# Performance work log

Hardware: AMD Instinct MI355X
Metric: run time of the kernel (lower is better)

The kernel has to match this reference:

```python
import jax, jax.numpy as jnp
import numpy as np

NEG_INF = -1e9  # stands in for the -inf diagonal mask of criss-cross attention
BN_EPS = 1e-5


def conv1x1(x, w, b=None):
    # x: [B,Cin,H,W], w: [Cout,Cin]
    y = jnp.einsum('bchw,oc->bohw', x, w)
    if b is not None:
        y = y + b[None, :, None, None]
    return y


def criss_cross(qf, kf, vf, q_w, q_b, k_w, k_b, v_w, v_b, gamma):
    # Criss-cross attention (CCNet): row + column affinity, joint softmax, aggregate.
    B, C, H, W = vf.shape
    q = conv1x1(qf, q_w, q_b)  # [B,Ci,H,W]
    k = conv1x1(kf, k_w, k_b)  # [B,Ci,H,W]
    v = conv1x1(vf, v_w, v_b)  # [B,C,H,W]
    # column-wise (along H) energy, with -inf on the self position (h == h')
    eH = jnp.einsum('bchw,bcHw->bhwH', q, k)
    eH = eH + NEG_INF * jnp.eye(H, dtype=eH.dtype)[:, None, :]  # [H,1,H] broadcasts over w
    # row-wise (along W) energy
    eW = jnp.einsum('bchw,bchW->bhwW', q, k)
    att = jax.nn.softmax(jnp.concatenate([eH, eW], axis=-1), axis=-1)  # [B,H,W,H+W]
    aH, aW = att[..., :H], att[..., H:]
    outH = jnp.einsum('bcHw,bhwH->bchw', v, aH)
    outW = jnp.einsum('bchW,bhwW->bchw', v, aW)
    return gamma * (outH + outW) + vf


def batchnorm(x, scale, bias):
    # training-mode BN over (N,H,W)
    mean = x.mean(axis=(0, 2, 3), keepdims=True)
    var = x.var(axis=(0, 2, 3), keepdims=True)
    xh = (x - mean) * jax.lax.rsqrt(var + BN_EPS)
    return xh * scale[None, :, None, None] + bias[None, :, None, None]


def setup_inputs() -> dict:
    key = jax.random.key(0)
    ks = jax.random.split(key, 16)
    B, C, H, W = 8, 512, 96, 96
    Hh, Wh = 48, 48
    Cin = C // 2    # 256
    Ci = C // 16    # 32
    s = 0.02
    inp = {
        'low_feature': jax.random.normal(ks[0], (B, C, H, W), jnp.float32),
        'high_feature': jax.random.normal(ks[1], (B, C, Hh, Wh), jnp.float32),
        'conv1_w': jax.random.normal(ks[2], (Cin, C), jnp.float32) * s,
        'conv1_b': jnp.zeros((Cin,), jnp.float32),
        'conv2_w': jax.random.normal(ks[3], (Cin, C), jnp.float32) * s,
        'conv2_b': jnp.zeros((Cin,), jnp.float32),
        'q_w': jax.random.normal(ks[4], (Ci, Cin), jnp.float32) * s,
        'q_b': jnp.zeros((Ci,), jnp.float32),
        'k_w': jax.random.normal(ks[5], (Ci, Cin), jnp.float32) * s,
        'k_b': jnp.zeros((Ci,), jnp.float32),
        'v_w': jax.random.normal(ks[6], (Cin, Cin), jnp.float32) * s,
        'v_b': jnp.zeros((Cin,), jnp.float32),
        'gamma': jnp.array(0.1, jnp.float32),
        'bottleneck_w': jax.random.normal(ks[7], (C, Cin + C), jnp.float32) * s,
        'bn_scale': jnp.ones((C,), jnp.float32),
        'bn_bias': jnp.zeros((C,), jnp.float32),
    }
    return inp


def reference(low_feature, high_feature, conv1_w, conv1_b, conv2_w, conv2_b,
              q_w, q_b, k_w, k_b, v_w, v_b, gamma, bottleneck_w, bn_scale, bn_bias):
    B, C, H, W = low_feature.shape
    hf = jax.image.resize(high_feature, (B, high_feature.shape[1], H, W), method='bilinear')
    qf = conv1x1(low_feature, conv1_w, conv1_b)   # [B,C/2,H,W]
    vf = conv1x1(hf, conv2_w, conv2_b)            # [B,C/2,H,W]
    for _ in range(2):  # module applies the same attention twice
        vf = criss_cross(qf, vf, vf, q_w, q_b, k_w, k_b, v_w, v_b, gamma)
    cat = jnp.concatenate([vf, hf], axis=1)       # [B, C/2 + C, H, W]
    out = conv1x1(cat, bottleneck_w)              # bias=False
    out = batchnorm(out, bn_scale, bn_bias)
    return jax.nn.relu(out)
```

## Files before the change

### kernel.cpp

```cpp
#include <hip/hip_runtime.h>
#include <hip/hip_bf16.h>

typedef __hip_bfloat16 bf16;
typedef __attribute__((ext_vector_type(8))) short short8;
typedef __attribute__((ext_vector_type(4))) float f32x4;

constexpr int kHW = 96 * 96;

__device__ __forceinline__ float b2f(bf16 x){ return __bfloat162float(x); }
__device__ __forceinline__ bf16  f2b(float x){ return __float2bfloat16(x); }
__device__ __forceinline__ unsigned short b2u(bf16 x){ return *(unsigned short*)&x; }

#define SW(r, g) ((r)*32 + ((((g) ^ (((r) >> 1) & 3))) << 3))


__global__ void k_zero(float* __restrict__ p){
  int i = blockIdx.x*256 + threadIdx.x;
  if (i < 1024) p[i] = 0.0f;
}

__global__ void k_cvt(const float* __restrict__ s, bf16* __restrict__ d, int n){
  int i = blockIdx.x*256 + threadIdx.x;
  if (i < n) d[i] = f2b(s[i]);
}

__global__ __launch_bounds__(256) void k_upsample(const float* __restrict__ hi,
                                                  bf16* __restrict__ hf_t){
  int y = blockIdx.x, b = blockIdx.y, t = threadIdx.x;
  int j = y >> 1;
  int j0, j1; float wy0, wy1;
  if ((y & 1) == 0){ j0 = j - 1; if (j0 < 0) j0 = 0; j1 = j; wy0 = 0.25f; wy1 = 0.75f; }
  else             { j0 = j; j1 = j + 1; if (j1 > 47) j1 = 47; wy0 = 0.75f; wy1 = 0.25f; }
  __shared__ __align__(16) float sm[2][128][49];
  for (int c0 = 0; c0 < 512; c0 += 128){
    for (int e = t; e < 2*128*48; e += 256){
      int cl = e / 96; int r = e % 96; int jj = r / 48; int i = r % 48;
      int row = jj ? j1 : j0;
      sm[jj][cl][i] = hi[(((size_t)b*512 + c0 + cl)*48 + row)*48 + i];
    }
    __syncthreads();
    for (int e = t; e < 96*128; e += 256){
      int x = e >> 7; int cl = e & 127;
      int i = x >> 1; int i0, i1; float wx0, wx1;
      if ((x & 1) == 0){ i0 = i - 1; if (i0 < 0) i0 = 0; i1 = i; wx0 = 0.25f; wx1 = 0.75f; }
      else             { i0 = i; i1 = i + 1; if (i1 > 47) i1 = 47; wx0 = 0.75f; wx1 = 0.25f; }
      float v = wy0*(wx0*sm[0][cl][i0] + wx1*sm[0][cl][i1])
              + wy1*(wx0*sm[1][cl][i0] + wx1*sm[1][cl][i1]);
      hf_t[(((size_t)b*96 + x)*96 + y)*512 + c0 + cl] = f2b(v);
    }
    __syncthreads();
  }
}

__global__ void k_qqw(const float* __restrict__ q_w, const float* __restrict__ c1_w,
                      bf16* __restrict__ qq_wb){
  int gid = blockIdx.x*256 + threadIdx.x;
  int o = gid >> 9, c = gid & 511;
  float acc = 0.f;
  for (int k = 0; k < 256; k++) acc += q_w[o*256 + k] * c1_w[k*512 + c];
  qq_wb[gid] = f2b(acc);
}
__global__ void k_qqb(const float* __restrict__ q_w, const float* __restrict__ c1_b,
                      const float* __restrict__ q_b, float* __restrict__ qq_b){
  int o = threadIdx.x; if (o >= 32) return;
  float acc = q_b[o];
  for (int k = 0; k < 256; k++) acc += q_w[o*256 + k] * c1_b[k];
  qq_b[o] = acc;
}

__global__ __launch_bounds__(256) void k_mfma_gemm(const bf16* __restrict__ A,
                                                   const bf16* __restrict__ Wb,
                                                   const float* __restrict__ bias,
                                                   bf16* __restrict__ out,
                                                   int K, int O){
  int b = blockIdx.z, n0 = blockIdx.x*128, o0 = blockIdx.y*128;
  int t = threadIdx.x, lane = t & 63, wv = t >> 6;
  int m_off = (wv & 1)*64, o_off = (wv >> 1)*64;
  int lm = lane & 15, lk = lane >> 4;
  __shared__ __align__(16) bf16 As[2][128*32];
  __shared__ __align__(16) bf16 Ws[2][128*32];
  f32x4 acc[4][4] = {};
  const bf16* Ab = A + (size_t)b*kHW*K;
  int nl0 = t >> 2, gp = t & 3, p0 = gp*8;
  uint4 pa0, pa1, pw0, pw1;
  pa0 = *(const uint4*)&Ab[(size_t)(n0+nl0)*K + p0];
  pa1 = *(const uint4*)&Ab[(size_t)(n0+nl0+64)*K + p0];
  pw0 = *(const uint4*)&Wb[(size_t)(o0+nl0)*K + p0];
  pw1 = *(const uint4*)&Wb[(size_t)(o0+nl0+64)*K + p0];
  *(uint4*)&As[0][SW(nl0, gp)]    = pa0;
  *(uint4*)&As[0][SW(nl0+64, gp)] = pa1;
  *(uint4*)&Ws[0][SW(nl0, gp)]    = pw0;
  *(uint4*)&Ws[0][SW(nl0+64, gp)] = pw1;
  int cur = 0;
  int NS = K >> 5;
  for (int s = 0; s < NS; s++){
    if (s+1 < NS){
      int c0 = (s+1)*32;
      pa0 = *(const uint4*)&Ab[(size_t)(n0+nl0)*K + c0 + p0];
      pa1 = *(const uint4*)&Ab[(size_t)(n0+nl0+64)*K + c0 + p0];
      pw0 = *(const uint4*)&Wb[(size_t)(o0+nl0)*K + c0 + p0];
      pw1 = *(const uint4*)&Wb[(size_t)(o0+nl0+64)*K + c0 + p0];
    }
    __syncthreads();
    short8 af[4], bfr[4];
    #pragma unroll
    for (int i = 0; i < 4; i++){
      af[i]  = *(const short8*)&As[cur][SW(m_off + i*16 + lm, lk)];
      bfr[i] = *(const short8*)&Ws[cur][SW(o_off + i*16 + lm, lk)];
    }
    #pragma unroll
    for (int i = 0; i < 4; i++)
      #pragma unroll
      for (int j = 0; j < 4; j++)
        acc[i][j] = __builtin_amdgcn_mfma_f32_16x16x32_bf16(af[i], bfr[j], acc[i][j], 0, 0, 0);
    if (s+1 < NS){
      int nx = cur ^ 1;
      *(uint4*)&As[nx][SW(nl0, gp)]    = pa0;
      *(uint4*)&As[nx][SW(nl0+64, gp)] = pa1;
      *(uint4*)&Ws[nx][SW(nl0, gp)]    = pw0;
      *(uint4*)&Ws[nx][SW(nl0+64, gp)] = pw1;
      cur = nx;
    }
  }
  #pragma unroll
  for (int j = 0; j < 4; j++){
    int oc = o0 + o_off + j*16 + lm;
    float bs = bias ? bias[oc] : 0.0f;
    #pragma unroll
    for (int i = 0; i < 4; i++){
      int rbase = n0 + m_off + i*16 + lk*4;
      #pragma unroll
      for (int r = 0; r < 4; r++)
        out[((size_t)b*kHW + rbase + r)*(size_t)O + oc] = f2b(acc[i][j][r] + bs);
    }
  }
}

__global__ __launch_bounds__(256) void k_bneck_mfma(const bf16* __restrict__ vf,
                                                    const bf16* __restrict__ hf,
                                                    const bf16* __restrict__ Wb,
                                                    bf16* __restrict__ out,
                                                    float* __restrict__ s1,
                                                    float* __restrict__ s2){
  int b = blockIdx.z, n0 = blockIdx.x*128, o0 = blockIdx.y*128;
  int t = threadIdx.x, lane = t & 63, wv = t >> 6;
  int m_off = (wv & 1)*64, o_off = (wv >> 1)*64;
  int lm = lane & 15, lk = lane >> 4;
  __shared__ __align__(16) bf16 As[2][128*32];
  __shared__ __align__(16) bf16 Ws[2][128*32];
  __shared__ float l1[128];
  __shared__ float l2[128];
  if (t < 128){ l1[t] = 0.f; l2[t] = 0.f; }
  f32x4 acc[4][4] = {};
  int nl0 = t >> 2, gp = t & 3, p0 = gp*8;
  const bf16* vfb = vf + (size_t)b*kHW*256;
  const bf16* hfb = hf + (size_t)b*kHW*512;
  uint4 pa0, pa1, pw0, pw1;
  pa0 = *(const uint4*)&vfb[(size_t)(n0+nl0)*256 + p0];
  pa1 = *(const uint4*)&vfb[(size_t)(n0+nl0+64)*256 + p0];
  pw0 = *(const uint4*)&Wb[(size_t)(o0+nl0)*768 + p0];
  pw1 = *(const uint4*)&Wb[(size_t)(o0+nl0+64)*768 + p0];
  *(uint4*)&As[0][SW(nl0, gp)]    = pa0;
  *(uint4*)&As[0][SW(nl0+64, gp)] = pa1;
  *(uint4*)&Ws[0][SW(nl0, gp)]    = pw0;
  *(uint4*)&Ws[0][SW(nl0+64, gp)] = pw1;
  int cur = 0;
  for (int s = 0; s < 24; s++){
    if (s+1 < 24){
      int c0 = (s+1)*32;
      if (c0 < 256){
        pa0 = *(const uint4*)&vfb[(size_t)(n0+nl0)*256 + c0 + p0];
        pa1 = *(const uint4*)&vfb[(size_t)(n0+nl0+64)*256 + c0 + p0];
      } else {
        int cc = c0 - 256;
        pa0 = *(const uint4*)&hfb[(size_t)(n0+nl0)*512 + cc + p0];
        pa1 = *(const uint4*)&hfb[(size_t)(n0+nl0+64)*512 + cc + p0];
      }
      pw0 = *(const uint4*)&Wb[(size_t)(o0+nl0)*768 + c0 + p0];
      pw1 = *(const uint4*)&Wb[(size_t)(o0+nl0+64)*768 + c0 + p0];
    }
    __syncthreads();
    short8 af[4], bfr[4];
    #pragma unroll
    for (int i = 0; i < 4; i++){
      af[i]  = *(const short8*)&As[cur][SW(m_off + i*16 + lm, lk)];
      bfr[i] = *(const short8*)&Ws[cur][SW(o_off + i*16 + lm, lk)];
    }
    #pragma unroll
    for (int i = 0; i < 4; i++)
      #pragma unroll
      for (int j = 0; j < 4; j++)
        acc[i][j] = __builtin_amdgcn_mfma_f32_16x16x32_bf16(af[i], bfr[j], acc[i][j], 0, 0, 0);
    if (s+1 < 24){
      int nx = cur ^ 1;
      *(uint4*)&As[nx][SW(nl0, gp)]    = pa0;
      *(uint4*)&As[nx][SW(nl0+64, gp)] = pa1;
      *(uint4*)&Ws[nx][SW(nl0, gp)]    = pw0;
      *(uint4*)&Ws[nx][SW(nl0+64, gp)] = pw1;
      cur = nx;
    }
  }
  #pragma unroll
  for (int j = 0; j < 4; j++){
    int oc = o0 + o_off + j*16 + lm;
    float p1 = 0.f, p2 = 0.f;
    #pragma unroll
    for (int i = 0; i < 4; i++){
      int rbase = n0 + m_off + i*16 + lk*4;
      #pragma unroll
      for (int r = 0; r < 4; r++){
        float v = acc[i][j][r];
        p1 += v; p2 += v*v;
        out[((size_t)b*kHW + rbase + r)*512 + oc] = f2b(v);
      }
    }
    int cl = o_off + j*16 + lm;
    atomicAdd(&l1[cl], p1);
    atomicAdd(&l2[cl], p2);
  }
  __syncthreads();
  if (t < 128){
    atomicAdd(&s1[o0 + t], l1[t]);
    atomicAdd(&s2[o0 + t], l2[t]);
  }
}

__global__ __launch_bounds__(256) void k_qmfma(const float* __restrict__ low,
                                               const bf16* __restrict__ qq_wb,
                                               const float* __restrict__ qq_b,
                                               bf16* __restrict__ q_t){
  int n0 = blockIdx.x*64, b = blockIdx.y, t = threadIdx.x;
  int lane = t & 63, wv = t >> 6;
  int m_off = wv*16;
  int lm = lane & 15, lk = lane >> 4;
  __shared__ __align__(16) bf16 As[64*36];
  __shared__ __align__(16) bf16 Ws[32*40];
  f32x4 acc[2] = {};
  const float* low_b = low + (size_t)b*512*kHW;
  int c2 = (t & 15)*2;
  int xg = t >> 4;
  for (int c0 = 0; c0 < 512; c0 += 32){
    const float* p0 = low_b + (size_t)(c0 + c2)*kHW + n0 + xg*4;
    float4 a0 = *(const float4*)p0;
    float4 a1 = *(const float4*)(p0 + kHW);
    float f0[4] = {a0.x, a0.y, a0.z, a0.w};
    float f1[4] = {a1.x, a1.y, a1.z, a1.w};
    #pragma unroll
    for (int u = 0; u < 4; u++){
      ushort2 pr;
      bf16 v0 = f2b(f0[u]), v1 = f2b(f1[u]);
      pr.x = b2u(v0); pr.y = b2u(v1);
      *(ushort2*)&As[(xg*4 + u)*36 + c2] = pr;
    }
    if (t < 128){
      int ol = t >> 2, p = t & 3;
      *(uint4*)&Ws[ol*40 + p*8] = *(const uint4*)&qq_wb[(size_t)ol*512 + c0 + p*8];
    }
    __syncthreads();
    short8 af = *(const short8*)&As[(m_off + lm)*36 + lk*8];
    short8 b0 = *(const short8*)&Ws[lm*40 + lk*8];
    short8 b1 = *(const short8*)&Ws[(16 + lm)*40 + lk*8];
    acc[0] = __builtin_amdgcn_mfma_f32_16x16x32_bf16(af, b0, acc[0], 0, 0, 0);
    acc[1] = __builtin_amdgcn_mfma_f32_16x16x32_bf16(af, b1, acc[1], 0, 0, 0);
    __syncthreads();
  }
  #pragma unroll
  for (int j = 0; j < 2; j++){
    int oc = j*16 + lm;
    float bs = qq_b[oc];
    #pragma unroll
    for (int r = 0; r < 4; r++){
      int ng = n0 + m_off + lk*4 + r;
      int h = ng / 96, x = ng - h*96;
      q_t[(((size_t)b*96 + x)*96 + h)*32 + oc] = f2b(acc[j][r] + bs);
    }
  }
}

__global__ __launch_bounds__(256) void k_kmfma(const bf16* __restrict__ A,
                                               const bf16* __restrict__ Wk,
                                               const float* __restrict__ bias,
                                               bf16* __restrict__ out){
  int n0 = blockIdx.x*128, b = blockIdx.y;
  int t = threadIdx.x, lane = t & 63, wv = t >> 6;
  int m_off = wv*32;
  int lm = lane & 15, lk = lane >> 4;
  __shared__ __align__(16) bf16 As[2][128*32];
  __shared__ __align__(16) bf16 Ws[2][32*32];
  f32x4 acc[2][2] = {};
  const bf16* Ab = A + (size_t)b*kHW*256;
  int nl0 = t >> 2, gp = t & 3, p0 = gp*8;
  int ol = t >> 2;
  uint4 pa0, pa1, pw;
  pa0 = *(const uint4*)&Ab[(size_t)(n0+nl0)*256 + p0];
  pa1 = *(const uint4*)&Ab[(size_t)(n0+nl0+64)*256 + p0];
  if (t < 128) pw = *(const uint4*)&Wk[(size_t)ol*256 + p0];
  *(uint4*)&As[0][SW(nl0, gp)]    = pa0;
  *(uint4*)&As[0][SW(nl0+64, gp)] = pa1;
  if (t < 128) *(uint4*)&Ws[0][SW(ol, gp)] = pw;
  int cur = 0;
  for (int s = 0; s < 8; s++){
    if (s+1 < 8){
      int c0 = (s+1)*32;
      pa0 = *(const uint4*)&Ab[(size_t)(n0+nl0)*256 + c0 + p0];
      pa1 = *(const uint4*)&Ab[(size_t)(n0+nl0+64)*256 + c0 + p0];
      if (t < 128) pw = *(const uint4*)&Wk[(size_t)ol*256 + c0 + p0];
    }
    __syncthreads();
    short8 af[2], bfr[2];
    #pragma unroll
    for (int i = 0; i < 2; i++)
      af[i] = *(const short8*)&As[cur][SW(m_off + i*16 + lm, lk)];
    #pragma unroll
    for (int j = 0; j < 2; j++)
      bfr[j] = *(const short8*)&Ws[cur][SW(j*16 + lm, lk)];
    #pragma unroll
    for (int i = 0; i < 2; i++)
      #pragma unroll
      for (int j = 0; j < 2; j++)
        acc[i][j] = __builtin_amdgcn_mfma_f32_16x16x32_bf16(af[i], bfr[j], acc[i][j], 0, 0, 0);
    if (s+1 < 8){
      int nx = cur ^ 1;
      *(uint4*)&As[nx][SW(nl0, gp)]    = pa0;
      *(uint4*)&As[nx][SW(nl0+64, gp)] = pa1;
      if (t < 128) *(uint4*)&Ws[nx][SW(ol, gp)] = pw;
      cur = nx;
    }
  }
  #pragma unroll
  for (int j = 0; j < 2; j++){
    int oc = j*16 + lm;
    float bs = bias[oc];
    #pragma unroll
    for (int i = 0; i < 2; i++){
      int rbase = n0 + m_off + i*16 + lk*4;
      #pragma unroll
      for (int r = 0; r < 4; r++)
        out[((size_t)b*kHW + rbase + r)*32 + oc] = f2b(acc[i][j][r] + bs);
    }
  }
}

__global__ __launch_bounds__(256) void k_eH(const bf16* __restrict__ q_t,
                                            const bf16* __restrict__ k_t,
                                            bf16* __restrict__ att){
  int w = blockIdx.x, b = blockIdx.y, t = threadIdx.x;
  __shared__ float Qs[96][33];
  __shared__ float Ks[96][33];
  const bf16* Qp = q_t + (((size_t)b*96 + w)*96)*32;
  const bf16* Kp = k_t + (((size_t)b*96 + w)*96)*32;
  for (int e = t; e < 3072; e += 256){ Qs[e>>5][e&31] = b2f(Qp[e]); Ks[e>>5][e&31] = b2f(Kp[e]); }
  __syncthreads();
  int tj = t % 16, th = t / 16;
  float acc[6][6] = {};
  #pragma unroll 4
  for (int c = 0; c < 32; c++){
    float qa[6], kb[6];
    #pragma unroll
    for (int i = 0; i < 6; i++) qa[i] = Qs[th*6 + i][c];
    #pragma unroll
    for (int jj = 0; jj < 6; jj++) kb[jj] = Ks[tj*6 + jj][c];
    #pragma unroll
    for (int i = 0; i < 6; i++)
      #pragma unroll
      for (int jj = 0; jj < 6; jj++) acc[i][jj] += qa[i]*kb[jj];
  }
  #pragma unroll
  for (int i = 0; i < 6; i++){
    int h = th*6 + i;
    size_t base = (((size_t)b*96 + h)*96 + w)*192;
    #pragma unroll
    for (int jj = 0; jj < 6; jj++){
      int jg = tj*6 + jj;
      float e = acc[i][jj];
      if (jg == h) e += -1000000000.0f;
      att[base + jg] = f2b(e);
    }
  }
}

__global__ __launch_bounds__(256) void k_eW(const bf16* __restrict__ q_t,
                                            const bf16* __restrict__ k_t,
                                            bf16* __restrict__ att){
  int h = blockIdx.x, b = blockIdx.y, t = threadIdx.x;
  __shared__ float Qs[96][33];
  __shared__ float Ks[96][33];
  for (int e = t; e < 3072; e += 256){
    int wl = e >> 5, c = e & 31;
    size_t idx = (((size_t)b*96 + wl)*96 + h)*32 + c;
    Qs[wl][c] = b2f(q_t[idx]);
    Ks[wl][c] = b2f(k_t[idx]);
  }
  __syncthreads();
  int tj = t % 16, tw = t / 16;
  float acc[6][6] = {};
  #pragma unroll 4
  for (int c = 0; c < 32; c++){
    float qa[6], kb[6];
    #pragma unroll
    for (int i = 0; i < 6; i++) qa[i] = Qs[tw*6 + i][c];
    #pragma unroll
    for (int jj = 0; jj < 6; jj++) kb[jj] = Ks[tj*6 + jj][c];
    #pragma unroll
    for (int i = 0; i < 6; i++)
      #pragma unroll
      for (int jj = 0; jj < 6; jj++) acc[i][jj] += qa[i]*kb[jj];
  }
  #pragma unroll
  for (int i = 0; i < 6; i++){
    int wl = tw*6 + i;
    size_t base = (((size_t)b*96 + h)*96 + wl)*192 + 96;
    #pragma unroll
    for (int jj = 0; jj < 6; jj++) att[base + tj*6 + jj] = f2b(acc[i][jj]);
  }
}

__global__ __launch_bounds__(256) void k_softmax(bf16* __restrict__ att){
  int t = threadIdx.x;
  int row = blockIdx.x*4 + (t >> 6);
  int lane = t & 63;
  size_t base = (size_t)row * 192;
  float x0 = b2f(att[base + lane]);
  float x1 = b2f(att[base + 64 + lane]);
  float x2 = b2f(att[base + 128 + lane]);
  float m = fmaxf(x0, fmaxf(x1, x2));
  #pragma unroll
  for (int off = 32; off; off >>= 1) m = fmaxf(m, __shfl_xor(m, off));
  float e0 = __expf(x0 - m), e1 = __expf(x1 - m), e2 = __expf(x2 - m);
  float s = e0 + e1 + e2;
  #pragma unroll
  for (int off = 32; off; off >>= 1) s += __shfl_xor(s, off);
  float inv = 1.0f / s;
  att[base + lane]       = f2b(e0 * inv);
  att[base + 64 + lane]  = f2b(e1 * inv);
  att[base + 128 + lane] = f2b(e2 * inv);
}

__global__ __launch_bounds__(256) void k_outH_mfma(const bf16* __restrict__ att,
                                                   const bf16* __restrict__ v_t,
                                                   bf16* __restrict__ accb){
  int w = blockIdx.x, b = blockIdx.y, t = threadIdx.x;
  int lane = t & 63, wv = t >> 6;
  int m_off = (wv & 1)*48, o_off = (wv >> 1)*128;
  int lm = lane & 15, lk = lane >> 4;
  __shared__ __align__(16) bf16 As[96*36];
  __shared__ __align__(16) bf16 Vt[256*36];
  f32x4 acc[3][8] = {};
  const bf16* Vb = v_t + ((size_t)b*96 + w)*96*256;
  for (int j0 = 0; j0 < 96; j0 += 32){
    for (int e = t; e < 384; e += 256){
      int h = e >> 2, p = e & 3;
      *(uint4*)&As[h*36 + p*8] =
        *(const uint4*)&att[(((size_t)b*96 + h)*96 + w)*192 + j0 + p*8];
    }
    for (int e = t; e < 512; e += 256){
      int jj2 = (e & 15)*2, cg = e >> 4;
      const bf16* p = Vb + (size_t)(j0 + jj2)*256 + cg*8;
      uint4 a0 = *(const uint4*)p;
      uint4 a1 = *(const uint4*)(p + 256);
      const unsigned short* u0 = (const unsigned short*)&a0;
      const unsigned short* u1 = (const unsigned short*)&a1;
      #pragma unroll
      for (int u = 0; u < 8; u++){
        ushort2 pr; pr.x = u0[u]; pr.y = u1[u];
        *(ushort2*)&Vt[(cg*8 + u)*36 + jj2] = pr;
      }
    }
    __syncthreads();
    short8 af[3], bfr[8];
    #pragma unroll
    for (int i = 0; i < 3; i++)
      af[i] = *(const short8*)&As[(m_off + i*16 + lm)*36 + lk*8];
    #pragma unroll
    for (int j = 0; j < 8; j++)
      bfr[j] = *(const short8*)&Vt[(o_off + j*16 + lm)*36 + lk*8];
    #pragma unroll
    for (int i = 0; i < 3; i++)
      #pragma unroll
      for (int j = 0; j < 8; j++)
        acc[i][j] = __builtin_amdgcn_mfma_f32_16x16x32_bf16(af[i], bfr[j], acc[i][j], 0, 0, 0);
    __syncthreads();
  }
  #pragma unroll
  for (int j = 0; j < 8; j++){
    int c = o_off + j*16 + lm;
    #pragma unroll
    for (int i = 0; i < 3; i++){
      int hbase = m_off + i*16 + lk*4;
      #pragma unroll
      for (int r = 0; r < 4; r++)
        accb[(((size_t)b*96 + w)*96 + hbase + r)*256 + c] = f2b(acc[i][j][r]);
    }
  }
}

__global__ __launch_bounds__(256) void k_outW_mfma(const bf16* __restrict__ att,
                                                   const bf16* __restrict__ v_t,
                                                   const bf16* __restrict__ accb,
                                                   const float* __restrict__ gamma_p,
                                                   bf16* __restrict__ vf_t){
  int h = blockIdx.x, b = blockIdx.y, t = threadIdx.x;
  int lane = t & 63, wv = t >> 6;
  int m_off = (wv & 1)*48, o_off = (wv >> 1)*128;
  int lm = lane & 15, lk = lane >> 4;
  __shared__ __align__(16) bf16 As[96*36];
  __shared__ __align__(16) bf16 Vt[256*36];
  f32x4 acc[3][8] = {};
  for (int j0 = 0; j0 < 96; j0 += 32){
    for (int e = t; e < 384; e += 256){
      int wl = e >> 2, p = e & 3;
      *(uint4*)&As[wl*36 + p*8] =
        *(const uint4*)&att[(((size_t)b*96 + h)*96 + wl)*192 + 96 + j0 + p*8];
    }
    for (int e = t; e < 512; e += 256){
      int jj2 = (e & 15)*2, cg = e >> 4;
      const bf16* p = v_t + (((size_t)b*96 + j0 + jj2)*96 + h)*256 + cg*8;
      uint4 a0 = *(const uint4*)p;
      uint4 a1 = *(const uint4*)(p + 96*256);
      const unsigned short* u0 = (const unsigned short*)&a0;
      const unsigned short* u1 = (const unsigned short*)&a1;
      #pragma unroll
      for (int u = 0; u < 8; u++){
        ushort2 pr; pr.x = u0[u]; pr.y = u1[u];
        *(ushort2*)&Vt[(cg*8 + u)*36 + jj2] = pr;
      }
    }
    __syncthreads();
    short8 af[3], bfr[8];
    #pragma unroll
    for (int i = 0; i < 3; i++)
      af[i] = *(const short8*)&As[(m_off + i*16 + lm)*36 + lk*8];
    #pragma unroll
    for (int j = 0; j < 8; j++)
      bfr[j] = *(const short8*)&Vt[(o_off + j*16 + lm)*36 + lk*8];
    #pragma unroll
    for (int i = 0; i < 3; i++)
      #pragma unroll
      for (int j = 0; j < 8; j++)
        acc[i][j] = __builtin_amdgcn_mfma_f32_16x16x32_bf16(af[i], bfr[j], acc[i][j], 0, 0, 0);
    __syncthreads();
  }
  float g = gamma_p[0];
  #pragma unroll
  for (int j = 0; j < 8; j++){
    int c = o_off + j*16 + lm;
    #pragma unroll
    for (int i = 0; i < 3; i++){
      int wbase = m_off + i*16 + lk*4;
      #pragma unroll
      for (int r = 0; r < 4; r++){
        size_t idx = (((size_t)b*96 + wbase + r)*96 + h)*256 + c;
        vf_t[idx] = f2b(b2f(vf_t[idx]) + g*(acc[i][j][r] + b2f(accb[idx])));
      }
    }
  }
}

__global__ void k_bnprep(const float* __restrict__ s1, const float* __restrict__ s2,
                         const float* __restrict__ sc, const float* __restrict__ bi,
                         float2* __restrict__ ab){
  int co = blockIdx.x*256 + threadIdx.x;
  if (co >= 512) return;
  const float N = 73728.0f;
  float mean = s1[co] / N;
  float var  = s2[co] / N - mean*mean;
  if (var < 0.f) var = 0.f;
  float a = rsqrtf(var + 1e-5f) * sc[co];
  ab[co] = make_float2(a, bi[co] - mean*a);
}

__global__ __launch_bounds__(256) void k_bnout(const bf16* __restrict__ bt,
                                               const float2* __restrict__ ab,
                                               float* __restrict__ out){
  int w0 = blockIdx.x*32, h = blockIdx.y, b = blockIdx.z, t = threadIdx.x;
  __shared__ float Tl[32][33];
  for (int co0 = 0; co0 < 512; co0 += 32){
    for (int e = t; e < 1024; e += 256){
      int wl = e >> 5, co = e & 31;
      Tl[wl][co] = b2f(bt[(((size_t)b*96 + w0 + wl)*96 + h)*512 + co0 + co]);
    }
    __syncthreads();
    for (int e = t; e < 1024; e += 256){
      int co = e >> 5, wl = e & 31;
      float2 s = ab[co0 + co];
      float v = fmaxf(Tl[wl][co]*s.x + s.y, 0.0f);
      out[(((size_t)b*512 + co0 + co)*96 + h)*96 + w0 + wl] = v;
    }
    __syncthreads();
  }
}

extern "C" void kernel_launch(void* const* d_in, const int* in_sizes, int n_in,
                              void* d_out, int out_size, void* d_ws, size_t ws_size,
                              hipStream_t stream){
  (void)in_sizes; (void)n_in; (void)out_size; (void)ws_size;
  const float* low   = (const float*)d_in[0];
  const float* high  = (const float*)d_in[1];
  const float* c1w   = (const float*)d_in[2];
  const float* c1b   = (const float*)d_in[3];
  const float* c2w   = (const float*)d_in[4];
  const float* c2b   = (const float*)d_in[5];
  const float* qw    = (const float*)d_in[6];
  const float* qb    = (const float*)d_in[7];
  const float* kw    = (const float*)d_in[8];
  const float* kb    = (const float*)d_in[9];
  const float* vw    = (const float*)d_in[10];
  const float* vb    = (const float*)d_in[11];
  const float* gamma = (const float*)d_in[12];
  const float* bw    = (const float*)d_in[13];
  const float* bns   = (const float*)d_in[14];
  const float* bnb   = (const float*)d_in[15];
  float* out = (float*)d_out;

  char* wsb = (char*)d_ws;
  bf16*   hf_t = (bf16*) (wsb + 0);
  bf16*   vf_t = (bf16*) (wsb + 75497472);
  bf16*   q_t  = (bf16*) (wsb + 113246208);
  bf16*   qq_wb= (bf16*) (wsb + 117964800);
  bf16*   wk   = (bf16*) (wsb + 117997568);
  float*  qq_b = (float*)(wsb + 118030336);
  float*  s1   = (float*)(wsb + 118030464);
  float*  s2   = (float*)(wsb + 118032512);
  float2* ab   = (float2*)(wsb + 118034560);
  bf16*   wbb  = (bf16*) (wsb + 118038656);
  bf16*   wc2  = (bf16*) (wsb + 118825088);
  bf16*   wv   = (bf16*) (wsb + 119087232);
  bf16*   v_t  = (bf16*) (wsb + 119218304);
  bf16*   att  = (bf16*) (wsb + 156967040);
  bf16*   accb = (bf16*) (wsb + 185278592);
  bf16*   k_t  = (bf16*) (wsb + 185278592);
  bf16*   bt   = (bf16*) (wsb + 119218304);

  k_zero<<<4, 256, 0, stream>>>(s1);
  k_cvt<<<1536, 256, 0, stream>>>(bw,  wbb, 393216);
  k_cvt<<<512,  256, 0, stream>>>(c2w, wc2, 131072);
  k_cvt<<<256,  256, 0, stream>>>(vw,  wv,  65536);
  k_cvt<<<32,   256, 0, stream>>>(kw,  wk,  8192);
  k_upsample<<<dim3(96, 8), 256, 0, stream>>>(high, hf_t);
  k_qqw<<<64, 256, 0, stream>>>(qw, c1w, qq_wb);
  k_qqb<<<1, 64, 0, stream>>>(qw, c1b, qb, qq_b);
  k_mfma_gemm<<<dim3(72, 2, 8), 256, 0, stream>>>(hf_t, wc2, c2b, vf_t, 512, 256);
  k_qmfma<<<dim3(144, 8), 256, 0, stream>>>(low, qq_wb, qq_b, q_t);

  for (int r = 0; r < 2; r++){
    k_kmfma<<<dim3(72, 8), 256, 0, stream>>>(vf_t, wk, kb, k_t);
    k_mfma_gemm<<<dim3(72, 2, 8), 256, 0, stream>>>(vf_t, wv, vb, v_t, 256, 256);
    k_eH<<<dim3(96, 8), 256, 0, stream>>>(q_t, k_t, att);
    k_eW<<<dim3(96, 8), 256, 0, stream>>>(q_t, k_t, att);
    k_softmax<<<18432, 256, 0, stream>>>(att);
    k_outH_mfma<<<dim3(96, 8), 256, 0, stream>>>(att, v_t, accb);
    k_outW_mfma<<<dim3(96, 8), 256, 0, stream>>>(att, v_t, accb, gamma, vf_t);
  }

  k_bneck_mfma<<<dim3(72, 4, 8), 256, 0, stream>>>(vf_t, hf_t, wbb, bt, s1, s2);
  k_bnprep<<<2, 256, 0, stream>>>(s1, s2, bns, bnb, ab);
  k_bnout<<<dim3(3, 96, 8), 256, 0, stream>>>(bt, ab, out);
}
```

Measured before the change: 956.3 us.

## Deepen GEMM prefetch pipeline and vectorize bf16 loads in attention and BN kernels

The two MFMA GEMM kernels now unroll the K loop by two with fixed LDS buffers, issuing global loads for A one stage further ahead than the W loads so more memory latency is hidden behind MFMA work. The eH/eW energy kernels switch from scalar bf16 loads to 16-byte short8 loads with bit-shift conversion into padded float4-aligned shared tiles. The BN output kernel loads 8 bf16 per thread with a uint4 and processes 64 channels per iteration. This costs more live registers for the prefetch buffers and changes the shared-memory padding, which could alter bank conflicts in the compute loops.

```diff
diff --git a/kernel.cpp b/kernel.cpp
--- a/kernel.cpp
+++ b/kernel.cpp
@@ -10,8 +10,19 @@
 __device__ __forceinline__ float b2f(bf16 x){ return __bfloat162float(x); }
 __device__ __forceinline__ bf16  f2b(float x){ return __float2bfloat16(x); }
 __device__ __forceinline__ unsigned short b2u(bf16 x){ return *(unsigned short*)&x; }
+__device__ __forceinline__ float s2f(short u){ return __uint_as_float(((unsigned)(unsigned short)u) << 16); }
 
 #define SW(r, g) ((r)*32 + ((((g) ^ (((r) >> 1) & 3))) << 3))
+
+#define MFMA_STEP(cb) do { \
+  short8 af_[4], bf_[4]; \
+  _Pragma("unroll") for (int i_ = 0; i_ < 4; i_++){ \
+    af_[i_] = *(const short8*)&As[cb][SW(m_off + i_*16 + lm, lk)]; \
+    bf_[i_] = *(const short8*)&Ws[cb][SW(o_off + i_*16 + lm, lk)]; } \
+  _Pragma("unroll") for (int i_ = 0; i_ < 4; i_++) \
+    _Pragma("unroll") for (int j_ = 0; j_ < 4; j_++) \
+      acc[i_][j_] = __builtin_amdgcn_mfma_f32_16x16x32_bf16(af_[i_], bf_[j_], acc[i_][j_], 0, 0, 0); \
+} while(0)
 
 
 __global__ void k_zero(float* __restrict__ p){
@@ -82,44 +93,43 @@
   f32x4 acc[4][4] = {};
   const bf16* Ab = A + (size_t)b*kHW*K;
   int nl0 = t >> 2, gp = t & 3, p0 = gp*8;
-  uint4 pa0, pa1, pw0, pw1;
-  pa0 = *(const uint4*)&Ab[(size_t)(n0+nl0)*K + p0];
-  pa1 = *(const uint4*)&Ab[(size_t)(n0+nl0+64)*K + p0];
-  pw0 = *(const uint4*)&Wb[(size_t)(o0+nl0)*K + p0];
-  pw1 = *(const uint4*)&Wb[(size_t)(o0+nl0+64)*K + p0];
-  *(uint4*)&As[0][SW(nl0, gp)]    = pa0;
-  *(uint4*)&As[0][SW(nl0+64, gp)] = pa1;
-  *(uint4*)&Ws[0][SW(nl0, gp)]    = pw0;
-  *(uint4*)&Ws[0][SW(nl0+64, gp)] = pw1;
-  int cur = 0;
+  const bf16* ar0 = Ab + (size_t)(n0+nl0)*K + p0;
+  const bf16* ar1 = Ab + (size_t)(n0+nl0+64)*K + p0;
+  const bf16* wr0 = Wb + (size_t)(o0+nl0)*K + p0;
+  const bf16* wr1 = Wb + (size_t)(o0+nl0+64)*K + p0;
   int NS = K >> 5;
-  for (int s = 0; s < NS; s++){
-    if (s+1 < NS){
-      int c0 = (s+1)*32;
-      pa0 = *(const uint4*)&Ab[(size_t)(n0+nl0)*K + c0 + p0];
-      pa1 = *(const uint4*)&Ab[(size_t)(n0+nl0+64)*K + c0 + p0];
-      pw0 = *(const uint4*)&Wb[(size_t)(o0+nl0)*K + c0 + p0];
-      pw1 = *(const uint4*)&Wb[(size_t)(o0+nl0+64)*K + c0 + p0];
-    }
-    __syncthreads();
-    short8 af[4], bfr[4];
-    #pragma unroll
-    for (int i = 0; i < 4; i++){
-      af[i]  = *(const short8*)&As[cur][SW(m_off + i*16 + lm, lk)];
-      bfr[i] = *(const short8*)&Ws[cur][SW(o_off + i*16 + lm, lk)];
-    }
-    #pragma unroll
-    for (int i = 0; i < 4; i++)
-      #pragma unroll
-      for (int j = 0; j < 4; j++)
-        acc[i][j] = __builtin_amdgcn_mfma_f32_16x16x32_bf16(af[i], bfr[j], acc[i][j], 0, 0, 0);
-    if (s+1 < NS){
-      int nx = cur ^ 1;
-      *(uint4*)&As[nx][SW(nl0, gp)]    = pa0;
-      *(uint4*)&As[nx][SW(nl0+64, gp)] = pa1;
-      *(uint4*)&Ws[nx][SW(nl0, gp)]    = pw0;
-      *(uint4*)&Ws[nx][SW(nl0+64, gp)] = pw1;
-      cur = nx;
+  {
+    uint4 t0 = *(const uint4*)ar0;
+    uint4 t1 = *(const uint4*)ar1;
+    uint4 t2 = *(const uint4*)wr0;
+    uint4 t3 = *(const uint4*)wr1;
+    *(uint4*)&As[0][SW(nl0, gp)]    = t0;
+    *(uint4*)&As[0][SW(nl0+64, gp)] = t1;
+    *(uint4*)&Ws[0][SW(nl0, gp)]    = t2;
+    *(uint4*)&Ws[0][SW(nl0+64, gp)] = t3;
+  }
+  uint4 Aa0, Aa1, Ab0, Ab1, Wx0, Wx1, Wy0, Wy1;
+  Aa0 = *(const uint4*)(ar0 + 32);
+  Aa1 = *(const uint4*)(ar1 + 32);
+  for (int s = 0; s < NS; s += 2){
+    if (s+2 < NS){ Ab0 = *(const uint4*)(ar0 + (s+2)*32); Ab1 = *(const uint4*)(ar1 + (s+2)*32); }
+    Wx0 = *(const uint4*)(wr0 + (s+1)*32);
+    Wx1 = *(const uint4*)(wr1 + (s+1)*32);
+    __syncthreads();
+    MFMA_STEP(0);
+    *(uint4*)&As[1][SW(nl0, gp)]    = Aa0;
+    *(uint4*)&As[1][SW(nl0+64, gp)] = Aa1;
+    *(uint4*)&Ws[1][SW(nl0, gp)]    = Wx0;
+    *(uint4*)&Ws[1][SW(nl0+64, gp)] = Wx1;
+    if (s+3 < NS){ Aa0 = *(const uint4*)(ar0 + (s+3)*32); Aa1 = *(const uint4*)(ar1 + (s+3)*32); }
+    if (s+2 < NS){ Wy0 = *(const uint4*)(wr0 + (s+2)*32); Wy1 = *(const uint4*)(wr1 + (s+2)*32); }
+    __syncthreads();
+    MFMA_STEP(1);
+    if (s+2 < NS){
+      *(uint4*)&As[0][SW(nl0, gp)]    = Ab0;
+      *(uint4*)&As[0][SW(nl0+64, gp)] = Ab1;
+      *(uint4*)&Ws[0][SW(nl0, gp)]    = Wy0;
+      *(uint4*)&Ws[0][SW(nl0+64, gp)] = Wy1;
     }
   }
   #pragma unroll
@@ -134,6 +144,13 @@
         out[((size_t)b*kHW + rbase + r)*(size_t)O + oc] = f2b(acc[i][j][r] + bs);
     }
   }
+}
+
+__device__ __forceinline__ const bf16* bneck_aptr(const bf16* vfb, const bf16* hfb,
+                                                  int nrow, int p0, int s){
+  int c0 = s*32;
+  return (c0 < 256) ? vfb + (size_t)nrow*256 + c0 + p0
+                    : hfb + (size_t)nrow*512 + (c0 - 256) + p0;
 }
 
 __global__ __launch_bounds__(256) void k_bneck_mfma(const bf16* __restrict__ vf,
@@ -155,49 +172,50 @@
   int nl0 = t >> 2, gp = t & 3, p0 = gp*8;
   const bf16* vfb = vf + (size_t)b*kHW*256;
   const bf16* hfb = hf + (size_t)b*kHW*512;
-  uint4 pa0, pa1, pw0, pw1;
-  pa0 = *(const uint4*)&vfb[(size_t)(n0+nl0)*256 + p0];
-  pa1 = *(const uint4*)&vfb[(size_t)(n0+nl0+64)*256 + p0];
-  pw0 = *(const uint4*)&Wb[(size_t)(o0+nl0)*768 + p0];
-  pw1 = *(const uint4*)&Wb[(size_t)(o0+nl0+64)*768 + p0];
-  *(uint4*)&As[0][SW(nl0, gp)]    = pa0;
-  *(uint4*)&As[0][SW(nl0+64, gp)] = pa1;
-  *(uint4*)&Ws[0][SW(nl0, gp)]    = pw0;
-  *(uint4*)&Ws[0][SW(nl0+64, gp)] = pw1;
-  int cur = 0;
-  for (int s = 0; s < 24; s++){
-    if (s+1 < 24){
-      int c0 = (s+1)*32;
-      if (c0 < 256){
-        pa0 = *(const uint4*)&vfb[(size_t)(n0+nl0)*256 + c0 + p0];
-        pa1 = *(const uint4*)&vfb[(size_t)(n0+nl0+64)*256 + c0 + p0];
-      } else {
-        int cc = c0 - 256;
-        pa0 = *(const uint4*)&hfb[(size_t)(n0+nl0)*512 + cc + p0];
-        pa1 = *(const uint4*)&hfb[(size_t)(n0+nl0+64)*512 + cc + p0];
-      }
-      pw0 = *(const uint4*)&Wb[(size_t)(o0+nl0)*768 + c0 + p0];
-      pw1 = *(const uint4*)&Wb[(size_t)(o0+nl0+64)*768 + c0 + p0];
-    }
-    __syncthreads();
-    short8 af[4], bfr[4];
-    #pragma unroll
-    for (int i = 0; i < 4; i++){
-      af[i]  = *(const short8*)&As[cur][SW(m_off + i*16 + lm, lk)];
-      bfr[i] = *(const short8*)&Ws[cur][SW(o_off + i*16 + lm, lk)];
-    }
-    #pragma unroll
-    for (int i = 0; i < 4; i++)
-      #pragma unroll
-      for (int j = 0; j < 4; j++)
-        acc[i][j] = __builtin_amdgcn_mfma_f32_16x16x32_bf16(af[i], bfr[j], acc[i][j], 0, 0, 0);
-    if (s+1 < 24){
-      int nx = cur ^ 1;
-      *(uint4*)&As[nx][SW(nl0, gp)]    = pa0;
-      *(uint4*)&As[nx][SW(nl0+64, gp)] = pa1;
-      *(uint4*)&Ws[nx][SW(nl0, gp)]    = pw0;
-      *(uint4*)&Ws[nx][SW(nl0+64, gp)] = pw1;
-      cur = nx;
+  const bf16* wr0 = Wb + (size_t)(o0+nl0)*768 + p0;
+  const bf16* wr1 = Wb + (size_t)(o0+nl0+64)*768 + p0;
+  int r0 = n0 + nl0, r1 = n0 + nl0 + 64;
+  {
+    uint4 t0 = *(const uint4*)bneck_aptr(vfb, hfb, r0, p0, 0);
+    uint4 t1 = *(const uint4*)bneck_aptr(vfb, hfb, r1, p0, 0);
+    uint4 t2 = *(const uint4*)wr0;
+    uint4 t3 = *(const uint4*)wr1;
+    *(uint4*)&As[0][SW(nl0, gp)]    = t0;
+    *(uint4*)&As[0][SW(nl0+64, gp)] = t1;
+    *(uint4*)&Ws[0][SW(nl0, gp)]    = t2;
+    *(uint4*)&Ws[0][SW(nl0+64, gp)] = t3;
+  }
+  uint4 Aa0, Aa1, Ab0, Ab1, Wx0, Wx1, Wy0, Wy1;
+  Aa0 = *(const uint4*)bneck_aptr(vfb, hfb, r0, p0, 1);
+  Aa1 = *(const uint4*)bneck_aptr(vfb, hfb, r1, p0, 1);
+  for (int s = 0; s < 24; s += 2){
+    if (s+2 < 24){
+      Ab0 = *(const uint4*)bneck_aptr(vfb, hfb, r0, p0, s+2);
+      Ab1 = *(const uint4*)bneck_aptr(vfb, hfb, r1, p0, s+2);
+    }
+    Wx0 = *(const uint4*)(wr0 + (s+1)*32);
+    Wx1 = *(const uint4*)(wr1 + (s+1)*32);
+    __syncthreads();
+    MFMA_STEP(0);
+    *(uint4*)&As[1][SW(nl0, gp)]    = Aa0;
+    *(uint4*)&As[1][SW(nl0+64, gp)] = Aa1;
+    *(uint4*)&Ws[1][SW(nl0, gp)]    = Wx0;
+    *(uint4*)&Ws[1][SW(nl0+64, gp)] = Wx1;
+    if (s+3 < 24){
+      Aa0 = *(const uint4*)bneck_aptr(vfb, hfb, r0, p0, s+3);
+      Aa1 = *(const uint4*)bneck_aptr(vfb, hfb, r1, p0, s+3);
+    }
+    if (s+2 < 24){
+      Wy0 = *(const uint4*)(wr0 + (s+2)*32);
+      Wy1 = *(const uint4*)(wr1 + (s+2)*32);
+    }
+    __syncthreads();
+    MFMA_STEP(1);
+    if (s+2 < 24){
+      *(uint4*)&As[0][SW(nl0, gp)]    = Ab0;
+      *(uint4*)&As[0][SW(nl0+64, gp)] = Ab1;
+      *(uint4*)&Ws[0][SW(nl0, gp)]    = Wy0;
+      *(uint4*)&Ws[0][SW(nl0+64, gp)] = Wy1;
     }
   }
   #pragma unroll
@@ -345,11 +363,23 @@
                                             const bf16* __restrict__ k_t,
                                             bf16* __restrict__ att){
   int w = blockIdx.x, b = blockIdx.y, t = threadIdx.x;
-  __shared__ float Qs[96][33];
-  __shared__ float Ks[96][33];
+  __shared__ __align__(16) float Qs[96][36];
+  __shared__ __align__(16) float Ks[96][36];
   const bf16* Qp = q_t + (((size_t)b*96 + w)*96)*32;
   const bf16* Kp = k_t + (((size_t)b*96 + w)*96)*32;
-  for (int e = t; e < 3072; e += 256){ Qs[e>>5][e&31] = b2f(Qp[e]); Ks[e>>5][e&31] = b2f(Kp[e]); }
+  for (int e = t; e < 384; e += 256){
+    int row = e >> 2, cg = (e & 3)*8;
+    short8 qv = *(const short8*)&Qp[row*32 + cg];
+    short8 kv = *(const short8*)&Kp[row*32 + cg];
+    float4 q0 = {s2f(qv[0]), s2f(qv[1]), s2f(qv[2]), s2f(qv[3])};
+    float4 q1 = {s2f(qv[4]), s2f(qv[5]), s2f(qv[6]), s2f(qv[7])};
+    float4 k0 = {s2f(kv[0]), s2f(kv[1]), s2f(kv[2]), s2f(kv[3])};
+    float4 k1 = {s2f(kv[4]), s2f(kv[5]), s2f(kv[6]), s2f(kv[7])};
+    *(float4*)&Qs[row][cg]     = q0;
+    *(float4*)&Qs[row][cg + 4] = q1;
+    *(float4*)&Ks[row][cg]     = k0;
+    *(float4*)&Ks[row][cg + 4] = k1;
+  }
   __syncthreads();
   int tj = t % 16, th = t / 16;
   float acc[6][6] = {};
@@ -383,13 +413,21 @@
                                             const bf16* __restrict__ k_t,
                                             bf16* __restrict__ att){
   int h = blockIdx.x, b = blockIdx.y, t = threadIdx.x;
-  __shared__ float Qs[96][33];
-  __shared__ float Ks[96][33];
-  for (int e = t; e < 3072; e += 256){
-    int wl = e >> 5, c = e & 31;
-    size_t idx = (((size_t)b*96 + wl)*96 + h)*32 + c;
-    Qs[wl][c] = b2f(q_t[idx]);
-    Ks[wl][c] = b2f(k_t[idx]);
+  __shared__ __align__(16) float Qs[96][36];
+  __shared__ __align__(16) float Ks[96][36];
+  for (int e = t; e < 384; e += 256){
+    int wl = e >> 2, cg = (e & 3)*8;
+    size_t idx = (((size_t)b*96 + wl)*96 + h)*32 + cg;
+    short8 qv = *(const short8*)&q_t[idx];
+    short8 kv = *(const short8*)&k_t[idx];
+    float4 q0 = {s2f(qv[0]), s2f(qv[1]), s2f(qv[2]), s2f(qv[3])};
+    float4 q1 = {s2f(qv[4]), s2f(qv[5]), s2f(qv[6]), s2f(qv[7])};
+    float4 k0 = {s2f(kv[0]), s2f(kv[1]), s2f(kv[2]), s2f(kv[3])};
+    float4 k1 = {s2f(kv[4]), s2f(kv[5]), s2f(kv[6]), s2f(kv[7])};
+    *(float4*)&Qs[wl][cg]     = q0;
+    *(float4*)&Qs[wl][cg + 4] = q1;
+    *(float4*)&Ks[wl][cg]     = k0;
+    *(float4*)&Ks[wl][cg + 4] = k1;
   }
   __syncthreads();
   int tj = t % 16, tw = t / 16;
@@ -573,14 +611,16 @@
                                                const float2* __restrict__ ab,
                                                float* __restrict__ out){
   int w0 = blockIdx.x*32, h = blockIdx.y, b = blockIdx.z, t = threadIdx.x;
-  __shared__ float Tl[32][33];
-  for (int co0 = 0; co0 < 512; co0 += 32){
-    for (int e = t; e < 1024; e += 256){
-      int wl = e >> 5, co = e & 31;
-      Tl[wl][co] = b2f(bt[(((size_t)b*96 + w0 + wl)*96 + h)*512 + co0 + co]);
-    }
-    __syncthreads();
-    for (int e = t; e < 1024; e += 256){
+  __shared__ float Tl[32][65];
+  int wl0 = t >> 3, cg0 = (t & 7)*8;
+  for (int co0 = 0; co0 < 512; co0 += 64){
+    uint4 d = *(const uint4*)&bt[(((size_t)b*96 + w0 + wl0)*96 + h)*512 + co0 + cg0];
+    const unsigned short* us = (const unsigned short*)&d;
+    #pragma unroll
+    for (int u = 0; u < 8; u++)
+      Tl[wl0][cg0 + u] = __uint_as_float(((unsigned)us[u]) << 16);
+    __syncthreads();
+    for (int e = t; e < 2048; e += 256){
       int co = e >> 5, wl = e & 31;
       float2 s = ab[co0 + co];
       float v = fmaxf(Tl[wl][co]*s.x + s.y, 0.0f);
```

New measurement: 943.0 us. About the same (-1.4%).
